# Optimization experiments

Hardware: AMD Instinct MI355X
Metric: run time of the kernel (lower is better)

The kernel has to match this reference:

```python
import jax, jax.numpy as jnp
import numpy as np

TAU = 2.0          # spikingjelly LIFNode default tau
V_TH = 1.0         # v_threshold
SG_ALPHA = 4.0     # surrogate sigmoid alpha (default)
B, T, C, V = 128, 2048, 3, 1
H, L, NC = 192, 2, 12


@jax.custom_vjp
def spike_fn(u):
    # Heaviside on (v - v_th); surrogate sigmoid gradient in bwd
    return (u >= 0.0).astype(u.dtype)

def _spike_fwd(u):
    return spike_fn(u), u

def _spike_bwd(u, g):
    s = jax.nn.sigmoid(SG_ALPHA * u)
    return (g * SG_ALPHA * s * (1.0 - s),)

spike_fn.defvjp(_spike_fwd, _spike_bwd)


def setup_inputs() -> dict:
    key = jax.random.key(0)
    ks = jax.random.split(key, 8)
    in_dim = C * V
    sc = lambda d: 1.0 / np.sqrt(d)
    return {
        "x": jax.random.normal(ks[0], (B, T, C, V), dtype=jnp.float32),
        "W_in": jax.random.uniform(ks[1], (H, in_dim), jnp.float32, -sc(in_dim), sc(in_dim)),
        "b_in": jax.random.uniform(ks[2], (H,), jnp.float32, -sc(in_dim), sc(in_dim)),
        "W_cells": jax.random.uniform(ks[3], (L, H, H), jnp.float32, -sc(H), sc(H)),
        "b_cells": jax.random.uniform(ks[4], (L, H), jnp.float32, -sc(H), sc(H)),
        "W_head": jax.random.uniform(ks[5], (NC, H), jnp.float32, -sc(H), sc(H)),
        "b_head": jax.random.uniform(ks[6], (NC,), jnp.float32, -sc(H), sc(H)),
    }


def reference(x, W_in, b_in, W_cells, b_cells, W_head, b_head):
    b, t = x.shape[0], x.shape[1]
    xf = x.reshape(b, t, -1)                               # [B,T,in_dim]
    # in_proj applied to every timestep up-front (one big GEMM)
    z_all = jnp.einsum('btd,hd->tbh', xf, W_in) + b_in     # [T,B,H]

    def step(carry, z_in):
        h, v = carry                                       # each [L,B,H]
        z = z_in
        new_h, new_v = [], []
        for l in range(L):
            z = z + h[l] @ W_cells[l].T + b_cells[l]
            v_l = v[l] + (z - v[l]) / TAU                  # LIF charge (decay_input)
            s = spike_fn(v_l - V_TH)                       # fire
            v_l = v_l * (1.0 - s)                          # hard reset to 0
            new_h.append(s)
            new_v.append(v_l)
            z = s
        return (jnp.stack(new_h), jnp.stack(new_v)), z

    init = (jnp.zeros((L, b, H), x.dtype), jnp.zeros((L, b, H), x.dtype))
    _, readout = jax.lax.scan(step, init, z_all)           # [T,B,H]
    feat = readout.mean(axis=0)                            # [B,H]; dropout is identity at eval
    return feat @ W_head.T + b_head                        # [B,NC]
```

## Files before the change

kernel.cpp:

```cpp
#include <hip/hip_runtime.h>

#define HN 192
#define TT 2048
#define NCLS 12
#define ROWB 768
#define L0_PAD    147456
#define LDS_LIST0 149504
#define LDS_LIST1 150784
#define LDS_S0    152064
#define LDS_FEAT  153600
#define LDS_TOTAL 154368

__global__ void snn_pack_k(const float* __restrict__ Wc, float* __restrict__ ws) {
  int idx = blockIdx.x * 256 + threadIdx.x;
  if (idx < HN * HN) {
    int i = idx / HN, j = idx % HN;
    ws[j * HN + i] = Wc[idx];
  } else if (idx < 2 * HN * HN) {
    int r = idx - HN * HN;
    int i = r / HN, j = r % HN;
    ws[(193 + j) * HN + i] = Wc[idx];
  } else {
    int r = idx - 2 * HN * HN;
    if (r < HN) ws[192 * HN + r] = 0.0f;
    if (r < 256) ws[385 * HN + r] = 0.0f;
  }
}

__device__ __forceinline__ float4 add4(float4 a, float4 b) {
  return make_float4(a.x + b.x, a.y + b.y, a.z + b.z, a.w + b.w);
}
__device__ __forceinline__ int lanecnt_lt(unsigned long long m) {
  return __builtin_amdgcn_mbcnt_hi((unsigned)(m >> 32),
           __builtin_amdgcn_mbcnt_lo((unsigned)m, 0u));
}

#define READC(da, db, base, c) do { \
  da = *(const int4*)((base) + (c) * 32); \
  db = *(const int4*)((base) + (c) * 32 + 16); } while (0)

#define ISS8Q(p, ca, cb, basep) do { \
  p##0 = *(const float4*)((basep) + (unsigned)(ca).x + ln16); \
  p##1 = *(const float4*)((basep) + (unsigned)(ca).y + ln16); \
  p##2 = *(const float4*)((basep) + (unsigned)(ca).z + ln16); \
  p##3 = *(const float4*)((basep) + (unsigned)(ca).w + ln16); \
  p##4 = *(const float4*)((basep) + (unsigned)(cb).x + ln16); \
  p##5 = *(const float4*)((basep) + (unsigned)(cb).y + ln16); \
  p##6 = *(const float4*)((basep) + (unsigned)(cb).z + ln16); \
  p##7 = *(const float4*)((basep) + (unsigned)(cb).w + ln16); } while (0)

#define CONS8Q(acc, p) acc = add4(acc, \
  add4(add4(add4(p##0, p##1), add4(p##2, p##3)), \
       add4(add4(p##4, p##5), add4(p##6, p##7))))

__global__ __launch_bounds__(128, 1) void snn_main_k(
    const float* __restrict__ x, const float* __restrict__ W_in,
    const float* __restrict__ b_in, const float* __restrict__ b_cells,
    const float* __restrict__ W_head, const float* __restrict__ b_head,
    const float* __restrict__ ws, float* __restrict__ out)
{
  extern __shared__ char lds[];
  const int tid = threadIdx.x;
  const int ln  = tid & 63;
  const bool isW0 = (tid < 64);
  const int b   = blockIdx.x;
  const unsigned ln16 = (unsigned)ln << 4;
  const char* ldsb = lds;
  char* list0b = lds + LDS_LIST0;
  char* list1b = lds + LDS_LIST1;
  float* feat  = (float*)(lds + LDS_FEAT);
  const char* w1zb = (const char*)ws + 192 * ROWB;

  {
    const float4* src = (const float4*)ws;
    float4* dst = (float4*)lds;
    for (int i = tid; i < (192 * ROWB) / 16; i += 128) dst[i] = src[i];
    ((float4*)(lds + L0_PAD))[tid] = make_float4(0.f, 0.f, 0.f, 0.f);
  }
  __syncthreads();

  int vz;
  asm volatile("v_mov_b32 %0, 0" : "=v"(vz));

  float wi0[4], wi1[4], wi2[4], zb[4], b1z[4];
  #pragma unroll
  for (int k = 0; k < 4; ++k) {
    int i = 4 * ln + k;
    bool a = (i < HN);
    int ii = a ? i : 0;
    wi0[k] = a ? W_in[ii * 3 + 0] : 0.f;
    wi1[k] = a ? W_in[ii * 3 + 1] : 0.f;
    wi2[k] = a ? W_in[ii * 3 + 2] : 0.f;
    zb[k]  = a ? (b_in[ii] + b_cells[ii]) : -1e30f;
    b1z[k] = a ? b_cells[HN + ii] : -1e30f;
  }
  const float* __restrict__ xb = x + (size_t)b * TT * 3;
  const int vo = ln * 3072;

  float v0k[4] = {0, 0, 0, 0};
  int n0 = 0;
  int4 c0a = {L0_PAD,L0_PAD,L0_PAD,L0_PAD}, c0b = c0a, c1a = c0a, c1b = c0a;
  float x0 = xb[vz + 0], x1 = xb[vz + 1], x2 = xb[vz + 2];
  float v1k[4] = {0, 0, 0, 0}, cntk[4] = {0, 0, 0, 0};
  int n1 = 0;
  float4 gA0, gA1, gA2, gA3, gA4, gA5, gA6, gA7;
  float4 gB0, gB1, gB2, gB3, gB4, gB5, gB6, gB7;
  if (!isW0) {
    int4 dz = {0, 0, 0, 0};
    ISS8Q(gA, dz, dz, w1zb);
    gB0=gB1=gB2=gB3=gB4=gB5=gB6=gB7=make_float4(0.f,0.f,0.f,0.f);
  }

  #pragma unroll 1
  for (int i = 0; i <= TT; ++i) {
    if (isW0) {
      if (i < TT) {
        const int wp = i & 1;
        float4 a0v = make_float4(0.f, 0.f, 0.f, 0.f);
        float4 hA0, hA1, hA2, hA3, hA4, hA5, hA6, hA7;
        float4 hB0, hB1, hB2, hB3, hB4, hB5, hB6, hB7;
        ISS8Q(hA, c0a, c0b, ldsb);
        if (n0 > 8) ISS8Q(hB, c1a, c1b, ldsb);
        float zarr[4];
        #pragma unroll
        for (int k = 0; k < 4; ++k)
          zarr[k] = x0 * wi0[k] + x1 * wi1[k] + x2 * wi2[k] + zb[k];
        const int tn = (i + 1 < TT) ? i + 1 : 0;
        const float nx0 = xb[tn * 3 + vz + 0];
        const float nx1 = xb[tn * 3 + vz + 1];
        const float nx2 = xb[tn * 3 + vz + 2];
        CONS8Q(a0v, hA);
        if (n0 > 8) CONS8Q(a0v, hB);
        if (n0 > 16) {
          int4 e2a, e2b;
          float4 r0, r1, r2, r3, r4, r5, r6, r7;
          READC(e2a, e2b, list0b, 2);
          ISS8Q(r, e2a, e2b, ldsb);
          CONS8Q(a0v, r);
          if (n0 > 24) {
            READC(e2a, e2b, list0b, 3);
            ISS8Q(r, e2a, e2b, ldsb);
            CONS8Q(a0v, r);
          }
          if (n0 > 32) {
            #pragma unroll 1
            for (int g = 4; g * 8 < n0; ++g) {
              READC(e2a, e2b, list0b, g);
              ISS8Q(r, e2a, e2b, ldsb);
              CONS8Q(a0v, r);
            }
          }
        }
        const float a0arr[4] = {a0v.x, a0v.y, a0v.z, a0v.w};
        float s0f[4];
        bool sp[4];
        unsigned long long mm0, mm1, mm2, mm3;
        {
          float u, v;
          u = zarr[0] + a0arr[0]; v = v0k[0] + (u - v0k[0]) * 0.5f;
          sp[0] = (v >= 1.0f); mm0 = __ballot(sp[0] ? 1 : 0);
          s0f[0] = sp[0] ? 1.0f : 0.0f; v0k[0] = sp[0] ? 0.0f : v;
          u = zarr[1] + a0arr[1]; v = v0k[1] + (u - v0k[1]) * 0.5f;
          sp[1] = (v >= 1.0f); mm1 = __ballot(sp[1] ? 1 : 0);
          s0f[1] = sp[1] ? 1.0f : 0.0f; v0k[1] = sp[1] ? 0.0f : v;
          u = zarr[2] + a0arr[2]; v = v0k[2] + (u - v0k[2]) * 0.5f;
          sp[2] = (v >= 1.0f); mm2 = __ballot(sp[2] ? 1 : 0);
          s0f[2] = sp[2] ? 1.0f : 0.0f; v0k[2] = sp[2] ? 0.0f : v;
          u = zarr[3] + a0arr[3]; v = v0k[3] + (u - v0k[3]) * 0.5f;
          sp[3] = (v >= 1.0f); mm3 = __ballot(sp[3] ? 1 : 0);
          s0f[3] = sp[3] ? 1.0f : 0.0f; v0k[3] = sp[3] ? 0.0f : v;
        }
        if (ln < 48)
          *(float4*)(lds + LDS_S0 + wp * 768 + ln16) =
              make_float4(s0f[0], s0f[1], s0f[2], s0f[3]);
        const int q0   = (int)__popcll(mm0);
        const int q01  = q0  + (int)__popcll(mm1);
        const int q012 = q01 + (int)__popcll(mm2);
        const int p0n  = q012 + (int)__popcll(mm3);
        const int jk = 256 + ln;
        {
          int s;
          s = sp[0] ? lanecnt_lt(mm0)          : jk; *(int*)(list0b + 4 * s) = vo;
          s = sp[1] ? (q0   + lanecnt_lt(mm1)) : jk; *(int*)(list0b + 4 * s) = vo + ROWB;
          s = sp[2] ? (q01  + lanecnt_lt(mm2)) : jk; *(int*)(list0b + 4 * s) = vo + 2 * ROWB;
          s = sp[3] ? (q012 + lanecnt_lt(mm3)) : jk; *(int*)(list0b + 4 * s) = vo + 3 * ROWB;
        }
        *(int*)(list0b + 4 * (p0n + ln)) = L0_PAD;
        n0 = p0n;
        asm volatile("" ::: "memory");
        READC(c0a, c0b, list0b, 0);
        READC(c1a, c1b, list0b, 1);
        asm volatile("s_waitcnt lgkmcnt(4)" ::: "memory");
        x0 = nx0; x1 = nx1; x2 = nx2;
      }
    } else {
      if (i > 0) {
        const int rp = (i - 1) & 1;
        const float4 s0v = *(const float4*)(lds + LDS_S0 + rp * 768 + ln16);
        float4 a1v = make_float4(0.f, 0.f, 0.f, 0.f);
        CONS8Q(a1v, gA);
        if (n1 > 8) CONS8Q(a1v, gB);
        if (n1 > 16) {
          int4 e2a, e2b;
          float4 r0, r1, r2, r3, r4, r5, r6, r7;
          READC(e2a, e2b, list1b, 2);
          ISS8Q(r, e2a, e2b, w1zb);
          CONS8Q(a1v, r);
          if (n1 > 24) {
            READC(e2a, e2b, list1b, 3);
            ISS8Q(r, e2a, e2b, w1zb);
            CONS8Q(a1v, r);
          }
          if (n1 > 32) {
            #pragma unroll 1
            for (int g = 4; g * 8 < n1; ++g) {
              READC(e2a, e2b, list1b, g);
              ISS8Q(r, e2a, e2b, w1zb);
              CONS8Q(a1v, r);
            }
          }
        }
        const float a1arr[4] = {a1v.x + s0v.x, a1v.y + s0v.y,
                                a1v.z + s0v.z, a1v.w + s0v.w};
        float s1w[4];
        bool sq[4];
        unsigned long long nn0, nn1, nn2, nn3;
        {
          float u, v;
          u = b1z[0] + a1arr[0]; v = v1k[0] + (u - v1k[0]) * 0.5f;
          sq[0] = (v >= 1.0f); nn0 = __ballot(sq[0] ? 1 : 0);
          s1w[0] = sq[0] ? 1.0f : 0.0f; v1k[0] = sq[0] ? 0.0f : v;
          u = b1z[1] + a1arr[1]; v = v1k[1] + (u - v1k[1]) * 0.5f;
          sq[1] = (v >= 1.0f); nn1 = __ballot(sq[1] ? 1 : 0);
          s1w[1] = sq[1] ? 1.0f : 0.0f; v1k[1] = sq[1] ? 0.0f : v;
          u = b1z[2] + a1arr[2]; v = v1k[2] + (u - v1k[2]) * 0.5f;
          sq[2] = (v >= 1.0f); nn2 = __ballot(sq[2] ? 1 : 0);
          s1w[2] = sq[2] ? 1.0f : 0.0f; v1k[2] = sq[2] ? 0.0f : v;
          u = b1z[3] + a1arr[3]; v = v1k[3] + (u - v1k[3]) * 0.5f;
          sq[3] = (v >= 1.0f); nn3 = __ballot(sq[3] ? 1 : 0);
          s1w[3] = sq[3] ? 1.0f : 0.0f; v1k[3] = sq[3] ? 0.0f : v;
        }
        cntk[0] += s1w[0]; cntk[1] += s1w[1]; cntk[2] += s1w[2]; cntk[3] += s1w[3];
        const int r0c  = (int)__popcll(nn0);
        const int r01  = r0c + (int)__popcll(nn1);
        const int r012 = r01 + (int)__popcll(nn2);
        const int p1n  = r012 + (int)__popcll(nn3);
        const int jk = 256 + ln;
        {
          int s;
          s = sq[0] ? lanecnt_lt(nn0)          : jk; *(int*)(list1b + 4 * s) = vo + ROWB;
          s = sq[1] ? (r0c  + lanecnt_lt(nn1)) : jk; *(int*)(list1b + 4 * s) = vo + 2 * ROWB;
          s = sq[2] ? (r01  + lanecnt_lt(nn2)) : jk; *(int*)(list1b + 4 * s) = vo + 3 * ROWB;
          s = sq[3] ? (r012 + lanecnt_lt(nn3)) : jk; *(int*)(list1b + 4 * s) = vo + 4 * ROWB;
        }
        *(int*)(list1b + 4 * (p1n + ln)) = 0;
        if (i < TT) {
          int4 d0a, d0b, d1a, d1b;
          asm volatile("" ::: "memory");
          READC(d0a, d0b, list1b, 0);
          READC(d1a, d1b, list1b, 1);
          ISS8Q(gA, d0a, d0b, w1zb);
          if (p1n > 8) ISS8Q(gB, d1a, d1b, w1zb);
        }
        n1 = p1n;
      }
    }
    asm volatile("" ::: "memory");
    __builtin_amdgcn_s_barrier();
    __builtin_amdgcn_sched_barrier(0);
    asm volatile("" ::: "memory");
  }

  __syncthreads();
  if (!isW0 && ln < 48) {
    const float r = 1.0f / 2048.0f;
    ((float4*)feat)[ln] = make_float4(cntk[0] * r, cntk[1] * r, cntk[2] * r, cntk[3] * r);
  }
  __syncthreads();
  if (tid < NCLS) {
    float a = b_head[tid];
    const float* wh = W_head + tid * HN;
    #pragma unroll 8
    for (int q = 0; q < HN; ++q) a += feat[q] * wh[q];
    out[b * NCLS + tid] = a;
  }
}

extern "C" void kernel_launch(void* const* d_in, const int* in_sizes, int n_in,
                              void* d_out, int out_size, void* d_ws, size_t ws_size,
                              hipStream_t stream) {
  const float* x       = (const float*)d_in[0];
  const float* W_in    = (const float*)d_in[1];
  const float* b_in    = (const float*)d_in[2];
  const float* W_cells = (const float*)d_in[3];
  const float* b_cells = (const float*)d_in[4];
  const float* W_head  = (const float*)d_in[5];
  const float* b_head  = (const float*)d_in[6];
  float* out = (float*)d_out;
  float* ws  = (float*)d_ws;

  snn_pack_k<<<(2 * HN * HN + 512 + 255) / 256, 256, 0, stream>>>(W_cells, ws);
  snn_main_k<<<128, 128, LDS_TOTAL, stream>>>(
      x, W_in, b_in, b_cells, W_head, b_head, ws, out);
}
```

Before: 891.5 us.

## Replace layer-0 LDS spike list with ballot-mask bit extraction and prefetched rows

Layer 0 no longer builds a compacted index list in LDS. It keeps the four spike ballot masks in scalar registers and extracts up to four firing neurons per mask with find-first-set. Their weight rows are issued as LDS loads right after the spike step, so they overlap the next iteration's input projection. Any remaining spikes are gathered in a serial bit-scan loop. The weight layout gains a zero row block at the front so empty slots read zeros. This removes the list write, read and barrier round-trip, but adds serial loads in the overflow loop when many neurons fire.

```diff
diff --git a/kernel.cpp b/kernel.cpp
--- a/kernel.cpp
+++ b/kernel.cpp
@@ -4,26 +4,26 @@
 #define TT 2048
 #define NCLS 12
 #define ROWB 768
-#define L0_PAD    147456
-#define LDS_LIST0 149504
-#define LDS_LIST1 150784
-#define LDS_S0    152064
-#define LDS_FEAT  153600
-#define LDS_TOTAL 154368
+#define LDS_S0    150528
+#define LDS_LIST1 152064
+#define LDS_FEAT  153344
+#define LDS_TOTAL 154112
+#define W1OFF 37632
 
 __global__ void snn_pack_k(const float* __restrict__ Wc, float* __restrict__ ws) {
-  int idx = blockIdx.x * 256 + threadIdx.x;
-  if (idx < HN * HN) {
-    int i = idx / HN, j = idx % HN;
-    ws[j * HN + i] = Wc[idx];
-  } else if (idx < 2 * HN * HN) {
-    int r = idx - HN * HN;
-    int i = r / HN, j = r % HN;
-    ws[(193 + j) * HN + i] = Wc[idx];
-  } else {
-    int r = idx - 2 * HN * HN;
-    if (r < HN) ws[192 * HN + r] = 0.0f;
-    if (r < 256) ws[385 * HN + r] = 0.0f;
+  int id = blockIdx.x * 256 + threadIdx.x;
+  if (id < 768) {
+    ws[id] = 0.0f;
+  } else if (id < 37632) {
+    int d = id - 768, j = d / 192, o = d % 192;
+    ws[(j + 4) * 192 + o] = Wc[o * 192 + j];
+  } else if (id < 37824) {
+    ws[id] = 0.0f;
+  } else if (id < 74688) {
+    int d = id - 37824, j = d / 192, o = d % 192;
+    ws[W1OFF + (j + 1) * 192 + o] = Wc[36864 + o * 192 + j];
+  } else if (id < 74944) {
+    ws[id - 74688 + 74880] = 0.0f;
   }
 }
 
@@ -33,6 +33,9 @@
 __device__ __forceinline__ int lanecnt_lt(unsigned long long m) {
   return __builtin_amdgcn_mbcnt_hi((unsigned)(m >> 32),
            __builtin_amdgcn_mbcnt_lo((unsigned)m, 0u));
+}
+__device__ __forceinline__ int ffs64(unsigned long long m) {
+  return __ffsll((long long)m) - 1;
 }
 
 #define READC(da, db, base, c) do { \
@@ -52,6 +55,8 @@
 #define CONS8Q(acc, p) acc = add4(acc, \
   add4(add4(add4(p##0, p##1), add4(p##2, p##3)), \
        add4(add4(p##4, p##5), add4(p##6, p##7))))
+
+#define EXT1(dst, m, wc) do { dst = ffs64(m) * 3072 + (wc); m &= m - 1; } while (0)
 
 __global__ __launch_bounds__(128, 1) void snn_main_k(
     const float* __restrict__ x, const float* __restrict__ W_in,
@@ -66,16 +71,14 @@
   const int b   = blockIdx.x;
   const unsigned ln16 = (unsigned)ln << 4;
   const char* ldsb = lds;
-  char* list0b = lds + LDS_LIST0;
   char* list1b = lds + LDS_LIST1;
   float* feat  = (float*)(lds + LDS_FEAT);
-  const char* w1zb = (const char*)ws + 192 * ROWB;
+  const char* w1zb = (const char*)ws + W1OFF * 4;
 
   {
     const float4* src = (const float4*)ws;
     float4* dst = (float4*)lds;
-    for (int i = tid; i < (192 * ROWB) / 16; i += 128) dst[i] = src[i];
-    ((float4*)(lds + L0_PAD))[tid] = make_float4(0.f, 0.f, 0.f, 0.f);
+    for (int i = tid; i < W1OFF / 4; i += 128) dst[i] = src[i];
   }
   __syncthreads();
 
@@ -98,8 +101,10 @@
   const int vo = ln * 3072;
 
   float v0k[4] = {0, 0, 0, 0};
-  int n0 = 0;
-  int4 c0a = {L0_PAD,L0_PAD,L0_PAD,L0_PAD}, c0b = c0a, c1a = c0a, c1b = c0a;
+  unsigned long long lm0 = 0, lm1 = 0, lm2 = 0, lm3 = 0;
+  float4 qq0,qq1,qq2,qq3,qq4,qq5,qq6,qq7,qq8,qq9,qq10,qq11,qq12,qq13,qq14,qq15;
+  qq0=qq1=qq2=qq3=qq4=qq5=qq6=qq7=make_float4(0.f,0.f,0.f,0.f);
+  qq8=qq9=qq10=qq11=qq12=qq13=qq14=qq15=qq0;
   float x0 = xb[vz + 0], x1 = xb[vz + 1], x2 = xb[vz + 2];
   float v1k[4] = {0, 0, 0, 0}, cntk[4] = {0, 0, 0, 0};
   int n1 = 0;
@@ -116,11 +121,21 @@
     if (isW0) {
       if (i < TT) {
         const int wp = i & 1;
-        float4 a0v = make_float4(0.f, 0.f, 0.f, 0.f);
-        float4 hA0, hA1, hA2, hA3, hA4, hA5, hA6, hA7;
-        float4 hB0, hB1, hB2, hB3, hB4, hB5, hB6, hB7;
-        ISS8Q(hA, c0a, c0b, ldsb);
-        if (n0 > 8) ISS8Q(hB, c1a, c1b, ldsb);
+        float4 a0v = add4(add4(add4(add4(qq0,qq1),add4(qq2,qq3)),
+                               add4(add4(qq4,qq5),add4(qq6,qq7))),
+                          add4(add4(add4(qq8,qq9),add4(qq10,qq11)),
+                               add4(add4(qq12,qq13),add4(qq14,qq15))));
+        if (lm0 | lm1 | lm2 | lm3) {
+          #pragma unroll 1
+          for (int w = 0; w < 4; ++w) {
+            unsigned long long m = (w==0)?lm0:(w==1)?lm1:(w==2)?lm2:lm3;
+            while (m) {
+              int off; EXT1(off, m, (w + 4) * 768);
+              a0v = add4(a0v, *(const float4*)(ldsb + (unsigned)off + ln16));
+            }
+          }
+          lm0 = lm1 = lm2 = lm3 = 0;
+        }
         float zarr[4];
         #pragma unroll
         for (int k = 0; k < 4; ++k)
@@ -129,68 +144,58 @@
         const float nx0 = xb[tn * 3 + vz + 0];
         const float nx1 = xb[tn * 3 + vz + 1];
         const float nx2 = xb[tn * 3 + vz + 2];
-        CONS8Q(a0v, hA);
-        if (n0 > 8) CONS8Q(a0v, hB);
-        if (n0 > 16) {
-          int4 e2a, e2b;
-          float4 r0, r1, r2, r3, r4, r5, r6, r7;
-          READC(e2a, e2b, list0b, 2);
-          ISS8Q(r, e2a, e2b, ldsb);
-          CONS8Q(a0v, r);
-          if (n0 > 24) {
-            READC(e2a, e2b, list0b, 3);
-            ISS8Q(r, e2a, e2b, ldsb);
-            CONS8Q(a0v, r);
-          }
-          if (n0 > 32) {
-            #pragma unroll 1
-            for (int g = 4; g * 8 < n0; ++g) {
-              READC(e2a, e2b, list0b, g);
-              ISS8Q(r, e2a, e2b, ldsb);
-              CONS8Q(a0v, r);
-            }
-          }
-        }
         const float a0arr[4] = {a0v.x, a0v.y, a0v.z, a0v.w};
         float s0f[4];
-        bool sp[4];
-        unsigned long long mm0, mm1, mm2, mm3;
+        unsigned long long M0, M1, M2, M3;
         {
           float u, v;
           u = zarr[0] + a0arr[0]; v = v0k[0] + (u - v0k[0]) * 0.5f;
-          sp[0] = (v >= 1.0f); mm0 = __ballot(sp[0] ? 1 : 0);
-          s0f[0] = sp[0] ? 1.0f : 0.0f; v0k[0] = sp[0] ? 0.0f : v;
+          bool s = (v >= 1.0f); M0 = __ballot(s ? 1 : 0);
+          s0f[0] = s ? 1.0f : 0.0f; v0k[0] = s ? 0.0f : v;
           u = zarr[1] + a0arr[1]; v = v0k[1] + (u - v0k[1]) * 0.5f;
-          sp[1] = (v >= 1.0f); mm1 = __ballot(sp[1] ? 1 : 0);
-          s0f[1] = sp[1] ? 1.0f : 0.0f; v0k[1] = sp[1] ? 0.0f : v;
+          bool s1 = (v >= 1.0f); M1 = __ballot(s1 ? 1 : 0);
+          s0f[1] = s1 ? 1.0f : 0.0f; v0k[1] = s1 ? 0.0f : v;
           u = zarr[2] + a0arr[2]; v = v0k[2] + (u - v0k[2]) * 0.5f;
-          sp[2] = (v >= 1.0f); mm2 = __ballot(sp[2] ? 1 : 0);
-          s0f[2] = sp[2] ? 1.0f : 0.0f; v0k[2] = sp[2] ? 0.0f : v;
+          bool s2 = (v >= 1.0f); M2 = __ballot(s2 ? 1 : 0);
+          s0f[2] = s2 ? 1.0f : 0.0f; v0k[2] = s2 ? 0.0f : v;
           u = zarr[3] + a0arr[3]; v = v0k[3] + (u - v0k[3]) * 0.5f;
-          sp[3] = (v >= 1.0f); mm3 = __ballot(sp[3] ? 1 : 0);
-          s0f[3] = sp[3] ? 1.0f : 0.0f; v0k[3] = sp[3] ? 0.0f : v;
+          bool s3 = (v >= 1.0f); M3 = __ballot(s3 ? 1 : 0);
+          s0f[3] = s3 ? 1.0f : 0.0f; v0k[3] = s3 ? 0.0f : v;
         }
         if (ln < 48)
           *(float4*)(lds + LDS_S0 + wp * 768 + ln16) =
               make_float4(s0f[0], s0f[1], s0f[2], s0f[3]);
-        const int q0   = (int)__popcll(mm0);
-        const int q01  = q0  + (int)__popcll(mm1);
-        const int q012 = q01 + (int)__popcll(mm2);
-        const int p0n  = q012 + (int)__popcll(mm3);
-        const int jk = 256 + ln;
+        asm volatile("" ::: "memory");
+        int of0,of1,of2,of3,of4,of5,of6,of7,of8,of9,of10,of11,of12,of13,of14,of15;
         {
-          int s;
-          s = sp[0] ? lanecnt_lt(mm0)          : jk; *(int*)(list0b + 4 * s) = vo;
-          s = sp[1] ? (q0   + lanecnt_lt(mm1)) : jk; *(int*)(list0b + 4 * s) = vo + ROWB;
-          s = sp[2] ? (q01  + lanecnt_lt(mm2)) : jk; *(int*)(list0b + 4 * s) = vo + 2 * ROWB;
-          s = sp[3] ? (q012 + lanecnt_lt(mm3)) : jk; *(int*)(list0b + 4 * s) = vo + 3 * ROWB;
-        }
-        *(int*)(list0b + 4 * (p0n + ln)) = L0_PAD;
-        n0 = p0n;
-        asm volatile("" ::: "memory");
-        READC(c0a, c0b, list0b, 0);
-        READC(c1a, c1b, list0b, 1);
-        asm volatile("s_waitcnt lgkmcnt(4)" ::: "memory");
+          unsigned long long m0 = M0, m1 = M1, m2 = M2, m3 = M3;
+          EXT1(of0,  m0, 3072); EXT1(of1,  m0, 3072);
+          EXT1(of2,  m0, 3072); EXT1(of3,  m0, 3072);
+          EXT1(of4,  m1, 3840); EXT1(of5,  m1, 3840);
+          EXT1(of6,  m1, 3840); EXT1(of7,  m1, 3840);
+          EXT1(of8,  m2, 4608); EXT1(of9,  m2, 4608);
+          EXT1(of10, m2, 4608); EXT1(of11, m2, 4608);
+          EXT1(of12, m3, 5376); EXT1(of13, m3, 5376);
+          EXT1(of14, m3, 5376); EXT1(of15, m3, 5376);
+          lm0 = m0; lm1 = m1; lm2 = m2; lm3 = m3;
+        }
+        qq0  = *(const float4*)(ldsb + (unsigned)of0  + ln16);
+        qq1  = *(const float4*)(ldsb + (unsigned)of1  + ln16);
+        qq2  = *(const float4*)(ldsb + (unsigned)of2  + ln16);
+        qq3  = *(const float4*)(ldsb + (unsigned)of3  + ln16);
+        qq4  = *(const float4*)(ldsb + (unsigned)of4  + ln16);
+        qq5  = *(const float4*)(ldsb + (unsigned)of5  + ln16);
+        qq6  = *(const float4*)(ldsb + (unsigned)of6  + ln16);
+        qq7  = *(const float4*)(ldsb + (unsigned)of7  + ln16);
+        qq8  = *(const float4*)(ldsb + (unsigned)of8  + ln16);
+        qq9  = *(const float4*)(ldsb + (unsigned)of9  + ln16);
+        qq10 = *(const float4*)(ldsb + (unsigned)of10 + ln16);
+        qq11 = *(const float4*)(ldsb + (unsigned)of11 + ln16);
+        qq12 = *(const float4*)(ldsb + (unsigned)of12 + ln16);
+        qq13 = *(const float4*)(ldsb + (unsigned)of13 + ln16);
+        qq14 = *(const float4*)(ldsb + (unsigned)of14 + ln16);
+        qq15 = *(const float4*)(ldsb + (unsigned)of15 + ln16);
+        asm volatile("s_waitcnt lgkmcnt(15)" ::: "memory");
         x0 = nx0; x1 = nx1; x2 = nx2;
       }
     } else {
@@ -299,7 +304,7 @@
   float* out = (float*)d_out;
   float* ws  = (float*)d_ws;
 
-  snn_pack_k<<<(2 * HN * HN + 512 + 255) / 256, 256, 0, stream>>>(W_cells, ws);
+  snn_pack_k<<<(74944 + 255) / 256, 256, 0, stream>>>(W_cells, ws);
   snn_main_k<<<128, 128, LDS_TOTAL, stream>>>(
       x, W_in, b_in, b_cells, W_head, b_head, ws, out);
 }
```

After: 1.169 ms. 1.31x slower.

## Replace per-step block barrier with LDS ring buffer and spin-wait counters

Applied to the files above, without the earlier changes.

The two wavefronts (layer 0 producer, layer 1 consumer) no longer meet at a block barrier every timestep. Layer-0 spikes go into an 8-slot LDS ring, and the two sides coordinate through volatile produce/consume counters, with the producer allowed to run up to 5 steps ahead. This decouples the two layers so one can absorb the other's variable per-step cost. The risks are spin-wait overhead, weak memory ordering on LDS (there is no explicit waitcnt/fence before publishing a counter), and the final head computation relying on feat written by the same wave.

```diff
diff --git a/kernel.cpp b/kernel.cpp
--- a/kernel.cpp
+++ b/kernel.cpp
@@ -5,11 +5,12 @@
 #define NCLS 12
 #define ROWB 768
 #define L0_PAD    147456
-#define LDS_LIST0 149504
-#define LDS_LIST1 150784
-#define LDS_S0    152064
-#define LDS_FEAT  153600
-#define LDS_TOTAL 154368
+#define LIST0     149504
+#define LIST1     150784
+#define RING      152064
+#define CNT       158208
+#define LDS_FEAT  158336
+#define LDS_TOTAL 159104
 
 __global__ void snn_pack_k(const float* __restrict__ Wc, float* __restrict__ ws) {
   int idx = blockIdx.x * 256 + threadIdx.x;
@@ -66,9 +67,11 @@
   const int b   = blockIdx.x;
   const unsigned ln16 = (unsigned)ln << 4;
   const char* ldsb = lds;
-  char* list0b = lds + LDS_LIST0;
-  char* list1b = lds + LDS_LIST1;
+  char* list0b = lds + LIST0;
+  char* list1b = lds + LIST1;
   float* feat  = (float*)(lds + LDS_FEAT);
+  volatile int* vprod = (volatile int*)(lds + CNT);
+  volatile int* vcons = (volatile int*)(lds + CNT + 64);
   const char* w1zb = (const char*)ws + 192 * ROWB;
 
   {
@@ -76,6 +79,7 @@
     float4* dst = (float4*)lds;
     for (int i = tid; i < (192 * ROWB) / 16; i += 128) dst[i] = src[i];
     ((float4*)(lds + L0_PAD))[tid] = make_float4(0.f, 0.f, 0.f, 0.f);
+    if (tid == 0) { *vprod = 0; *vcons = 0; }
   }
   __syncthreads();
 
@@ -97,192 +101,197 @@
   const float* __restrict__ xb = x + (size_t)b * TT * 3;
   const int vo = ln * 3072;
 
-  float v0k[4] = {0, 0, 0, 0};
-  int n0 = 0;
-  int4 c0a = {L0_PAD,L0_PAD,L0_PAD,L0_PAD}, c0b = c0a, c1a = c0a, c1b = c0a;
-  float x0 = xb[vz + 0], x1 = xb[vz + 1], x2 = xb[vz + 2];
-  float v1k[4] = {0, 0, 0, 0}, cntk[4] = {0, 0, 0, 0};
-  int n1 = 0;
-  float4 gA0, gA1, gA2, gA3, gA4, gA5, gA6, gA7;
-  float4 gB0, gB1, gB2, gB3, gB4, gB5, gB6, gB7;
-  if (!isW0) {
-    int4 dz = {0, 0, 0, 0};
-    ISS8Q(gA, dz, dz, w1zb);
-    gB0=gB1=gB2=gB3=gB4=gB5=gB6=gB7=make_float4(0.f,0.f,0.f,0.f);
-  }
-
-  #pragma unroll 1
-  for (int i = 0; i <= TT; ++i) {
-    if (isW0) {
-      if (i < TT) {
-        const int wp = i & 1;
-        float4 a0v = make_float4(0.f, 0.f, 0.f, 0.f);
-        float4 hA0, hA1, hA2, hA3, hA4, hA5, hA6, hA7;
-        float4 hB0, hB1, hB2, hB3, hB4, hB5, hB6, hB7;
-        ISS8Q(hA, c0a, c0b, ldsb);
-        if (n0 > 8) ISS8Q(hB, c1a, c1b, ldsb);
-        float zarr[4];
-        #pragma unroll
-        for (int k = 0; k < 4; ++k)
-          zarr[k] = x0 * wi0[k] + x1 * wi1[k] + x2 * wi2[k] + zb[k];
-        const int tn = (i + 1 < TT) ? i + 1 : 0;
-        const float nx0 = xb[tn * 3 + vz + 0];
-        const float nx1 = xb[tn * 3 + vz + 1];
-        const float nx2 = xb[tn * 3 + vz + 2];
-        CONS8Q(a0v, hA);
-        if (n0 > 8) CONS8Q(a0v, hB);
-        if (n0 > 16) {
-          int4 e2a, e2b;
-          float4 r0, r1, r2, r3, r4, r5, r6, r7;
-          READC(e2a, e2b, list0b, 2);
+  if (isW0) {
+    float v0k[4] = {0, 0, 0, 0};
+    int n0 = 0, cons_seen = 0;
+    int4 c0a = {L0_PAD,L0_PAD,L0_PAD,L0_PAD}, c0b = c0a, c1a = c0a, c1b = c0a;
+    float x0 = xb[vz + 0], x1 = xb[vz + 1], x2 = xb[vz + 2];
+
+    #pragma unroll 1
+    for (int i = 0; i < TT; ++i) {
+      if (i - cons_seen > 5) {
+        cons_seen = *vcons;
+        while (i - cons_seen > 5) cons_seen = *vcons;
+      }
+      float4 a0v = make_float4(0.f, 0.f, 0.f, 0.f);
+      float4 hA0, hA1, hA2, hA3, hA4, hA5, hA6, hA7;
+      float4 hB0, hB1, hB2, hB3, hB4, hB5, hB6, hB7;
+      ISS8Q(hA, c0a, c0b, ldsb);
+      if (n0 > 8) ISS8Q(hB, c1a, c1b, ldsb);
+      float zarr[4];
+      #pragma unroll
+      for (int k = 0; k < 4; ++k)
+        zarr[k] = x0 * wi0[k] + x1 * wi1[k] + x2 * wi2[k] + zb[k];
+      const int tn = (i + 1 < TT) ? i + 1 : 0;
+      const float nx0 = xb[tn * 3 + vz + 0];
+      const float nx1 = xb[tn * 3 + vz + 1];
+      const float nx2 = xb[tn * 3 + vz + 2];
+      CONS8Q(a0v, hA);
+      if (n0 > 8) CONS8Q(a0v, hB);
+      if (n0 > 16) {
+        int4 e2a, e2b;
+        float4 r0, r1, r2, r3, r4, r5, r6, r7;
+        READC(e2a, e2b, list0b, 2);
+        ISS8Q(r, e2a, e2b, ldsb);
+        CONS8Q(a0v, r);
+        if (n0 > 24) {
+          READC(e2a, e2b, list0b, 3);
           ISS8Q(r, e2a, e2b, ldsb);
           CONS8Q(a0v, r);
-          if (n0 > 24) {
-            READC(e2a, e2b, list0b, 3);
+        }
+        if (n0 > 32) {
+          #pragma unroll 1
+          for (int g = 4; g * 8 < n0; ++g) {
+            READC(e2a, e2b, list0b, g);
             ISS8Q(r, e2a, e2b, ldsb);
             CONS8Q(a0v, r);
           }
-          if (n0 > 32) {
-            #pragma unroll 1
-            for (int g = 4; g * 8 < n0; ++g) {
-              READC(e2a, e2b, list0b, g);
-              ISS8Q(r, e2a, e2b, ldsb);
-              CONS8Q(a0v, r);
-            }
-          }
         }
-        const float a0arr[4] = {a0v.x, a0v.y, a0v.z, a0v.w};
-        float s0f[4];
-        bool sp[4];
-        unsigned long long mm0, mm1, mm2, mm3;
-        {
-          float u, v;
-          u = zarr[0] + a0arr[0]; v = v0k[0] + (u - v0k[0]) * 0.5f;
-          sp[0] = (v >= 1.0f); mm0 = __ballot(sp[0] ? 1 : 0);
-          s0f[0] = sp[0] ? 1.0f : 0.0f; v0k[0] = sp[0] ? 0.0f : v;
-          u = zarr[1] + a0arr[1]; v = v0k[1] + (u - v0k[1]) * 0.5f;
-          sp[1] = (v >= 1.0f); mm1 = __ballot(sp[1] ? 1 : 0);
-          s0f[1] = sp[1] ? 1.0f : 0.0f; v0k[1] = sp[1] ? 0.0f : v;
-          u = zarr[2] + a0arr[2]; v = v0k[2] + (u - v0k[2]) * 0.5f;
-          sp[2] = (v >= 1.0f); mm2 = __ballot(sp[2] ? 1 : 0);
-          s0f[2] = sp[2] ? 1.0f : 0.0f; v0k[2] = sp[2] ? 0.0f : v;
-          u = zarr[3] + a0arr[3]; v = v0k[3] + (u - v0k[3]) * 0.5f;
-          sp[3] = (v >= 1.0f); mm3 = __ballot(sp[3] ? 1 : 0);
-          s0f[3] = sp[3] ? 1.0f : 0.0f; v0k[3] = sp[3] ? 0.0f : v;
-        }
-        if (ln < 48)
-          *(float4*)(lds + LDS_S0 + wp * 768 + ln16) =
-              make_float4(s0f[0], s0f[1], s0f[2], s0f[3]);
-        const int q0   = (int)__popcll(mm0);
-        const int q01  = q0  + (int)__popcll(mm1);
-        const int q012 = q01 + (int)__popcll(mm2);
-        const int p0n  = q012 + (int)__popcll(mm3);
-        const int jk = 256 + ln;
-        {
-          int s;
-          s = sp[0] ? lanecnt_lt(mm0)          : jk; *(int*)(list0b + 4 * s) = vo;
-          s = sp[1] ? (q0   + lanecnt_lt(mm1)) : jk; *(int*)(list0b + 4 * s) = vo + ROWB;
-          s = sp[2] ? (q01  + lanecnt_lt(mm2)) : jk; *(int*)(list0b + 4 * s) = vo + 2 * ROWB;
-          s = sp[3] ? (q012 + lanecnt_lt(mm3)) : jk; *(int*)(list0b + 4 * s) = vo + 3 * ROWB;
-        }
-        *(int*)(list0b + 4 * (p0n + ln)) = L0_PAD;
-        n0 = p0n;
-        asm volatile("" ::: "memory");
-        READC(c0a, c0b, list0b, 0);
-        READC(c1a, c1b, list0b, 1);
-        asm volatile("s_waitcnt lgkmcnt(4)" ::: "memory");
-        x0 = nx0; x1 = nx1; x2 = nx2;
-      }
-    } else {
-      if (i > 0) {
-        const int rp = (i - 1) & 1;
-        const float4 s0v = *(const float4*)(lds + LDS_S0 + rp * 768 + ln16);
-        float4 a1v = make_float4(0.f, 0.f, 0.f, 0.f);
-        CONS8Q(a1v, gA);
-        if (n1 > 8) CONS8Q(a1v, gB);
-        if (n1 > 16) {
-          int4 e2a, e2b;
-          float4 r0, r1, r2, r3, r4, r5, r6, r7;
-          READC(e2a, e2b, list1b, 2);
+      }
+      const float a0arr[4] = {a0v.x, a0v.y, a0v.z, a0v.w};
+      float s0f[4];
+      bool sp[4];
+      unsigned long long mm0, mm1, mm2, mm3;
+      {
+        float u, v;
+        u = zarr[0] + a0arr[0]; v = v0k[0] + (u - v0k[0]) * 0.5f;
+        sp[0] = (v >= 1.0f); mm0 = __ballot(sp[0] ? 1 : 0);
+        s0f[0] = sp[0] ? 1.0f : 0.0f; v0k[0] = sp[0] ? 0.0f : v;
+        u = zarr[1] + a0arr[1]; v = v0k[1] + (u - v0k[1]) * 0.5f;
+        sp[1] = (v >= 1.0f); mm1 = __ballot(sp[1] ? 1 : 0);
+        s0f[1] = sp[1] ? 1.0f : 0.0f; v0k[1] = sp[1] ? 0.0f : v;
+        u = zarr[2] + a0arr[2]; v = v0k[2] + (u - v0k[2]) * 0.5f;
+        sp[2] = (v >= 1.0f); mm2 = __ballot(sp[2] ? 1 : 0);
+        s0f[2] = sp[2] ? 1.0f : 0.0f; v0k[2] = sp[2] ? 0.0f : v;
+        u = zarr[3] + a0arr[3]; v = v0k[3] + (u - v0k[3]) * 0.5f;
+        sp[3] = (v >= 1.0f); mm3 = __ballot(sp[3] ? 1 : 0);
+        s0f[3] = sp[3] ? 1.0f : 0.0f; v0k[3] = sp[3] ? 0.0f : v;
+      }
+      if (ln < 48)
+        *(float4*)(lds + RING + ((i & 7) * 768) + ln16) =
+            make_float4(s0f[0], s0f[1], s0f[2], s0f[3]);
+      asm volatile("" ::: "memory");
+      if (ln == 0) *vprod = i + 1;
+      const int q0   = (int)__popcll(mm0);
+      const int q01  = q0  + (int)__popcll(mm1);
+      const int q012 = q01 + (int)__popcll(mm2);
+      const int p0n  = q012 + (int)__popcll(mm3);
+      const int jk = 256 + ln;
+      {
+        int s;
+        s = sp[0] ? lanecnt_lt(mm0)          : jk; *(int*)(list0b + 4 * s) = vo;
+        s = sp[1] ? (q0   + lanecnt_lt(mm1)) : jk; *(int*)(list0b + 4 * s) = vo + ROWB;
+        s = sp[2] ? (q01  + lanecnt_lt(mm2)) : jk; *(int*)(list0b + 4 * s) = vo + 2 * ROWB;
+        s = sp[3] ? (q012 + lanecnt_lt(mm3)) : jk; *(int*)(list0b + 4 * s) = vo + 3 * ROWB;
+      }
+      *(int*)(list0b + 4 * (p0n + ln)) = L0_PAD;
+      n0 = p0n;
+      asm volatile("" ::: "memory");
+      READC(c0a, c0b, list0b, 0);
+      READC(c1a, c1b, list0b, 1);
+      x0 = nx0; x1 = nx1; x2 = nx2;
+    }
+  } else {
+    float v1k[4] = {0, 0, 0, 0}, cntk[4] = {0, 0, 0, 0};
+    int n1 = 0, prod_seen = 0;
+    float4 gA0, gA1, gA2, gA3, gA4, gA5, gA6, gA7;
+    float4 gB0, gB1, gB2, gB3, gB4, gB5, gB6, gB7;
+    {
+      int4 dz = {0, 0, 0, 0};
+      ISS8Q(gA, dz, dz, w1zb);
+      gB0=gB1=gB2=gB3=gB4=gB5=gB6=gB7=make_float4(0.f,0.f,0.f,0.f);
+    }
+
+    #pragma unroll 1
+    for (int i = 0; i < TT; ++i) {
+      if (prod_seen <= i) {
+        do { prod_seen = *vprod; } while (prod_seen <= i);
+      }
+      asm volatile("" ::: "memory");
+      const float4 s0v = *(const float4*)(lds + RING + ((i & 7) * 768) + ln16);
+      float4 a1v = make_float4(0.f, 0.f, 0.f, 0.f);
+      CONS8Q(a1v, gA);
+      if (n1 > 8) CONS8Q(a1v, gB);
+      if (n1 > 16) {
+        int4 e2a, e2b;
+        float4 r0, r1, r2, r3, r4, r5, r6, r7;
+        READC(e2a, e2b, list1b, 2);
+        ISS8Q(r, e2a, e2b, w1zb);
+        CONS8Q(a1v, r);
+        if (n1 > 24) {
+          READC(e2a, e2b, list1b, 3);
           ISS8Q(r, e2a, e2b, w1zb);
           CONS8Q(a1v, r);
-          if (n1 > 24) {
-            READC(e2a, e2b, list1b, 3);
+        }
+        if (n1 > 32) {
+          #pragma unroll 1
+          for (int g = 4; g * 8 < n1; ++g) {
+            READC(e2a, e2b, list1b, g);
             ISS8Q(r, e2a, e2b, w1zb);
             CONS8Q(a1v, r);
           }
-          if (n1 > 32) {
-            #pragma unroll 1
-            for (int g = 4; g * 8 < n1; ++g) {
-              READC(e2a, e2b, list1b, g);
-              ISS8Q(r, e2a, e2b, w1zb);
-              CONS8Q(a1v, r);
-            }
-          }
         }
-        const float a1arr[4] = {a1v.x + s0v.x, a1v.y + s0v.y,
-                                a1v.z + s0v.z, a1v.w + s0v.w};
-        float s1w[4];
-        bool sq[4];
-        unsigned long long nn0, nn1, nn2, nn3;
-        {
-          float u, v;
-          u = b1z[0] + a1arr[0]; v = v1k[0] + (u - v1k[0]) * 0.5f;
-          sq[0] = (v >= 1.0f); nn0 = __ballot(sq[0] ? 1 : 0);
-          s1w[0] = sq[0] ? 1.0f : 0.0f; v1k[0] = sq[0] ? 0.0f : v;
-          u = b1z[1] + a1arr[1]; v = v1k[1] + (u - v1k[1]) * 0.5f;
-          sq[1] = (v >= 1.0f); nn1 = __ballot(sq[1] ? 1 : 0);
-          s1w[1] = sq[1] ? 1.0f : 0.0f; v1k[1] = sq[1] ? 0.0f : v;
-          u = b1z[2] + a1arr[2]; v = v1k[2] + (u - v1k[2]) * 0.5f;
-          sq[2] = (v >= 1.0f); nn2 = __ballot(sq[2] ? 1 : 0);
-          s1w[2] = sq[2] ? 1.0f : 0.0f; v1k[2] = sq[2] ? 0.0f : v;
-          u = b1z[3] + a1arr[3]; v = v1k[3] + (u - v1k[3]) * 0.5f;
-          sq[3] = (v >= 1.0f); nn3 = __ballot(sq[3] ? 1 : 0);
-          s1w[3] = sq[3] ? 1.0f : 0.0f; v1k[3] = sq[3] ? 0.0f : v;
-        }
-        cntk[0] += s1w[0]; cntk[1] += s1w[1]; cntk[2] += s1w[2]; cntk[3] += s1w[3];
-        const int r0c  = (int)__popcll(nn0);
-        const int r01  = r0c + (int)__popcll(nn1);
-        const int r012 = r01 + (int)__popcll(nn2);
-        const int p1n  = r012 + (int)__popcll(nn3);
-        const int jk = 256 + ln;
-        {
-          int s;
-          s = sq[0] ? lanecnt_lt(nn0)          : jk; *(int*)(list1b + 4 * s) = vo + ROWB;
-          s = sq[1] ? (r0c  + lanecnt_lt(nn1)) : jk; *(int*)(list1b + 4 * s) = vo + 2 * ROWB;
-          s = sq[2] ? (r01  + lanecnt_lt(nn2)) : jk; *(int*)(list1b + 4 * s) = vo + 3 * ROWB;
-          s = sq[3] ? (r012 + lanecnt_lt(nn3)) : jk; *(int*)(list1b + 4 * s) = vo + 4 * ROWB;
-        }
-        *(int*)(list1b + 4 * (p1n + ln)) = 0;
-        if (i < TT) {
-          int4 d0a, d0b, d1a, d1b;
-          asm volatile("" ::: "memory");
-          READC(d0a, d0b, list1b, 0);
-          READC(d1a, d1b, list1b, 1);
-          ISS8Q(gA, d0a, d0b, w1zb);
-          if (p1n > 8) ISS8Q(gB, d1a, d1b, w1zb);
-        }
-        n1 = p1n;
-      }
+      }
+      const float a1arr[4] = {a1v.x + s0v.x, a1v.y + s0v.y,
+                              a1v.z + s0v.z, a1v.w + s0v.w};
+      float s1w[4];
+      bool sq[4];
+      unsigned long long nn0, nn1, nn2, nn3;
+      {
+        float u, v;
+        u = b1z[0] + a1arr[0]; v = v1k[0] + (u - v1k[0]) * 0.5f;
+        sq[0] = (v >= 1.0f); nn0 = __ballot(sq[0] ? 1 : 0);
+        s1w[0] = sq[0] ? 1.0f : 0.0f; v1k[0] = sq[0] ? 0.0f : v;
+        u = b1z[1] + a1arr[1]; v = v1k[1] + (u - v1k[1]) * 0.5f;
+        sq[1] = (v >= 1.0f); nn1 = __ballot(sq[1] ? 1 : 0);
+        s1w[1] = sq[1] ? 1.0f : 0.0f; v1k[1] = sq[1] ? 0.0f : v;
+        u = b1z[2] + a1arr[2]; v = v1k[2] + (u - v1k[2]) * 0.5f;
+        sq[2] = (v >= 1.0f); nn2 = __ballot(sq[2] ? 1 : 0);
+        s1w[2] = sq[2] ? 1.0f : 0.0f; v1k[2] = sq[2] ? 0.0f : v;
+        u = b1z[3] + a1arr[3]; v = v1k[3] + (u - v1k[3]) * 0.5f;
+        sq[3] = (v >= 1.0f); nn3 = __ballot(sq[3] ? 1 : 0);
+        s1w[3] = sq[3] ? 1.0f : 0.0f; v1k[3] = sq[3] ? 0.0f : v;
+      }
+      cntk[0] += s1w[0]; cntk[1] += s1w[1]; cntk[2] += s1w[2]; cntk[3] += s1w[3];
+      const int r0c  = (int)__popcll(nn0);
+      const int r01  = r0c + (int)__popcll(nn1);
+      const int r012 = r01 + (int)__popcll(nn2);
+      const int p1n  = r012 + (int)__popcll(nn3);
+      const int jk = 256 + ln;
+      {
+        int s;
+        s = sq[0] ? lanecnt_lt(nn0)          : jk; *(int*)(list1b + 4 * s) = vo + ROWB;
+        s = sq[1] ? (r0c  + lanecnt_lt(nn1)) : jk; *(int*)(list1b + 4 * s) = vo + 2 * ROWB;
+        s = sq[2] ? (r01  + lanecnt_lt(nn2)) : jk; *(int*)(list1b + 4 * s) = vo + 3 * ROWB;
+        s = sq[3] ? (r012 + lanecnt_lt(nn3)) : jk; *(int*)(list1b + 4 * s) = vo + 4 * ROWB;
+      }
+      *(int*)(list1b + 4 * (p1n + ln)) = 0;
+      if (i + 1 < TT) {
+        int4 d0a, d0b, d1a, d1b;
+        asm volatile("" ::: "memory");
+        READC(d0a, d0b, list1b, 0);
+        READC(d1a, d1b, list1b, 1);
+        ISS8Q(gA, d0a, d0b, w1zb);
+        if (p1n > 8) ISS8Q(gB, d1a, d1b, w1zb);
+      }
+      n1 = p1n;
+      asm volatile("" ::: "memory");
+      if (ln == 0) *vcons = i + 1;
+    }
+
+    if (ln < 48) {
+      const float r = 1.0f / 2048.0f;
+      ((float4*)feat)[ln] =
+          make_float4(cntk[0] * r, cntk[1] * r, cntk[2] * r, cntk[3] * r);
     }
     asm volatile("" ::: "memory");
-    __builtin_amdgcn_s_barrier();
-    __builtin_amdgcn_sched_barrier(0);
-    asm volatile("" ::: "memory");
-  }
-
-  __syncthreads();
-  if (!isW0 && ln < 48) {
-    const float r = 1.0f / 2048.0f;
-    ((float4*)feat)[ln] = make_float4(cntk[0] * r, cntk[1] * r, cntk[2] * r, cntk[3] * r);
-  }
-  __syncthreads();
-  if (tid < NCLS) {
-    float a = b_head[tid];
-    const float* wh = W_head + tid * HN;
-    #pragma unroll 8
-    for (int q = 0; q < HN; ++q) a += feat[q] * wh[q];
-    out[b * NCLS + tid] = a;
+    if (ln < NCLS) {
+      float a = b_head[ln];
+      const float* wh = W_head + ln * HN;
+      #pragma unroll 8
+      for (int q = 0; q < HN; ++q) a += feat[q] * wh[q];
+      out[b * NCLS + ln] = a;
+    }
   }
 }
 
```

Result: slower. 1.033 ms (+15.9%).
